# Kernel optimization log

Measured on AMD Instinct MI355X. Metric: run time of the kernel, lower is better.

## Reference

```python
import jax, jax.numpy as jnp
import numpy as np

D_K = 128
SCALE = float(np.sqrt(D_K))

def setup_inputs() -> dict:
    key = jax.random.key(0)
    k1, k2, k3, k4 = jax.random.split(key, 4)
    B, S, D = 16, 2048, 128
    Q = jax.random.normal(k1, (B, S, D), dtype=jnp.float32)
    K = jax.random.normal(k2, (B, S, D), dtype=jnp.float32)
    V = jax.random.normal(k3, (B, S, D), dtype=jnp.float32)
    mask = jax.random.randint(k4, (B, 1, S), 0, 2).astype(jnp.bool_)
    return {"Q": Q, "K": K, "V": V, "mask": mask}

def reference(Q, K, V, mask):
    # scores: (B, Sq, Sk)
    scores = jnp.einsum("bqd,bkd->bqk", Q, K) / SCALE
    allow = jnp.broadcast_to(mask, scores.shape)
    neg = jnp.finfo(scores.dtype).min
    scores = jnp.where(allow, scores, neg)
    query_has_keys = jnp.any(allow, axis=-1, keepdims=True)  # (B, Sq, 1)
    scores = jnp.where(query_has_keys, scores, 0.0)
    attn_weights = jax.nn.softmax(scores, axis=-1)
    attn_weights = jnp.where(allow, attn_weights, 0.0)
    # dropout p=0.0 -> identity
    output = jnp.einsum("bqk,bkd->bqd", attn_weights, V)
    output = jnp.where(query_has_keys, output, 0.0)
    return output, attn_weights
```

## Files before the change

kernel.cpp:

```cpp
#include <hip/hip_runtime.h>

#define BB 16
#define SS 2048
#define DD 128
#define CE (0.08838834764831845f * 1.4426950408889634f)

typedef __attribute__((ext_vector_type(4))) float f32x4;
typedef __attribute__((ext_vector_type(8))) short short8;
typedef __attribute__((ext_vector_type(4))) unsigned short us4;
typedef __attribute__((ext_vector_type(8))) unsigned short us8;

__device__ inline unsigned short f2bf(float f) {
    unsigned u = __float_as_uint(f);
    u += 0x7fffu + ((u >> 16) & 1u);
    return (unsigned short)(u >> 16);
}

__device__ inline int swzA(int row, int col) {
    int byteoff = (row << 8) + ((col >> 3) << 4);
    byteoff ^= (row & 7) << 4;
    return (byteoff >> 1) + (col & 7);
}
__device__ inline int swzB(int row, int col) {
    int byteoff = (row << 7) + ((col >> 3) << 4);
    byteoff ^= (row & 7) << 4;
    return (byteoff >> 1) + (col & 7);
}

__global__ __launch_bounds__(256) void conv_bf16_kernel(
    const float* __restrict__ Q, const float* __restrict__ K,
    const int* __restrict__ mask,
    unsigned short* __restrict__ Qb, unsigned short* __restrict__ Kb,
    float* __restrict__ maskAdd)
{
    int idx = blockIdx.x * blockDim.x + threadIdx.x;
    const int total = BB * SS * DD / 4;
    for (int i = idx; i < total; i += gridDim.x * blockDim.x) {
        f32x4 q = reinterpret_cast<const f32x4*>(Q)[i];
        f32x4 k = reinterpret_cast<const f32x4*>(K)[i];
        us4 qh, kh;
        for (int j = 0; j < 4; ++j) { qh[j] = f2bf(q[j]); kh[j] = f2bf(k[j]); }
        reinterpret_cast<us4*>(Qb)[i] = qh;
        reinterpret_cast<us4*>(Kb)[i] = kh;
    }
    if (idx < BB * SS)
        maskAdd[idx] = mask[idx] ? 0.0f : __int_as_float(0xff800000);
}

__global__ __launch_bounds__(256) void vt_kernel(
    const float* __restrict__ V, unsigned short* __restrict__ VT)
{
    __shared__ unsigned short tile[64 * 136];
    int b = blockIdx.y, k0 = blockIdx.x << 6;
    int t = threadIdx.x;
    const float* Vg = V + ((size_t)b * SS + k0) * DD;
    for (int i = 0; i < 8; ++i) {
        int f4 = (i << 8) + t;
        int k  = f4 >> 5;
        int n  = (f4 & 31) << 2;
        f32x4 v = reinterpret_cast<const f32x4*>(Vg)[f4];
        us4 h;
        for (int j = 0; j < 4; ++j) h[j] = f2bf(v[j]);
        *reinterpret_cast<us4*>(&tile[k * 136 + n]) = h;
    }
    __syncthreads();
    unsigned short* outp = VT + (size_t)b * DD * SS;
    for (int i = 0; i < 4; ++i) {
        int id = (i << 8) + t;
        int n  = id >> 3;
        int c8 = id & 7;
        us8 o;
        for (int j = 0; j < 8; ++j) o[j] = tile[((c8 << 3) + j) * 136 + n];
        *reinterpret_cast<us8*>(&outp[(size_t)n * SS + k0 + (c8 << 3)]) = o;
    }
}

__global__ __launch_bounds__(256, 2) void flashA_kernel(
    const unsigned short* __restrict__ Qb, const unsigned short* __restrict__ Kb,
    const unsigned short* __restrict__ VT, const float* __restrict__ maskAdd,
    float* __restrict__ Op0, float* __restrict__ Op1, float* __restrict__ Lp)
{
    __shared__ unsigned short Ks[64 * 128];
    __shared__ unsigned short VTs[128 * 64];
    __shared__ unsigned short Ps[4 * 32 * 64];

    const int id = blockIdx.x;
    const int xcd = id & 7, j = id >> 3;
    const int b   = (xcd << 1) | (j >> 5);
    const int rem = j & 31;
    const int half = rem >> 4, qb = rem & 15;
    const int q0 = qb << 7;
    const int kvbase = half << 10;

    const int t = threadIdx.x, lane = t & 63, w = t >> 6;
    const int lr = lane & 15, lg = lane >> 4;

    const unsigned short* Kbb = Kb + (size_t)b * SS * DD;
    const unsigned short* Vbb = VT + (size_t)b * DD * SS;
    const float* Mb = maskAdd + (size_t)b * SS;

    const unsigned short* Qp = Qb + ((size_t)b * SS + q0 + w * 32) * DD;
    short8 qf[2][4];
    for (int m = 0; m < 2; ++m)
        for (int kb = 0; kb < 4; ++kb)
            qf[m][kb] = *reinterpret_cast<const short8*>(
                Qp + (size_t)(m * 16 + lr) * DD + kb * 32 + lg * 8);

    f32x4 oacc[2][8] = {};
    float rsum[2] = {0.f, 0.f};
    unsigned short* Pw = &Ps[w * 2048];

    us8 kstg[4], vstg[4];
    {
        for (int i = 0; i < 4; ++i) {
            int f = i * 256 + t;
            kstg[i] = *reinterpret_cast<const us8*>(
                Kbb + (size_t)(kvbase + (f >> 4)) * DD + ((f & 15) << 3));
            vstg[i] = *reinterpret_cast<const us8*>(
                Vbb + (size_t)(f >> 3) * SS + kvbase + ((f & 7) << 3));
        }
    }

    for (int kt = 0; kt < 16; ++kt) {
        const int kv0 = kvbase + (kt << 6);
        __syncthreads();
        for (int i = 0; i < 4; ++i) {
            int f = i * 256 + t;
            *reinterpret_cast<us8*>(&Ks[swzA(f >> 4, (f & 15) << 3)]) = kstg[i];
            *reinterpret_cast<us8*>(&VTs[swzB(f >> 3, (f & 7) << 3)]) = vstg[i];
        }
        __syncthreads();
        if (kt + 1 < 16) {
            int nb = kv0 + 64;
            for (int i = 0; i < 4; ++i) {
                int f = i * 256 + t;
                kstg[i] = *reinterpret_cast<const us8*>(
                    Kbb + (size_t)(nb + (f >> 4)) * DD + ((f & 15) << 3));
                vstg[i] = *reinterpret_cast<const us8*>(
                    Vbb + (size_t)(f >> 3) * SS + nb + ((f & 7) << 3));
            }
        }

        f32x4 sacc[2][4] = {};
        for (int kb = 0; kb < 4; ++kb) {
            short8 kf[4];
            for (int n = 0; n < 4; ++n)
                kf[n] = *reinterpret_cast<const short8*>(
                    &Ks[swzA(n * 16 + lr, kb * 32 + lg * 8)]);
            for (int n = 0; n < 4; ++n)
                for (int m = 0; m < 2; ++m)
                    sacc[m][n] = __builtin_amdgcn_mfma_f32_16x16x32_bf16(
                        kf[n], qf[m][kb], sacc[m][n], 0, 0, 0);
        }

        for (int n = 0; n < 4; ++n) {
            f32x4 ma = *reinterpret_cast<const f32x4*>(Mb + kv0 + n * 16 + lg * 4);
            for (int m = 0; m < 2; ++m) {
                us4 h;
                for (int r = 0; r < 4; ++r) {
                    float p = __builtin_amdgcn_exp2f(fmaf(sacc[m][n][r], CE, ma[r]));
                    rsum[m] += p;
                    h[r] = f2bf(p);
                }
                *reinterpret_cast<us4*>(&Pw[swzB(m * 16 + lr, n * 16 + lg * 4)]) = h;
            }
        }
        asm volatile("s_waitcnt lgkmcnt(0)" ::: "memory");
        __builtin_amdgcn_sched_barrier(0);

        for (int k2 = 0; k2 < 2; ++k2) {
            short8 pf[2];
            for (int m = 0; m < 2; ++m)
                pf[m] = *reinterpret_cast<const short8*>(
                    &Pw[swzB(m * 16 + lr, k2 * 32 + lg * 8)]);
            for (int nd = 0; nd < 8; ++nd) {
                short8 vf = *reinterpret_cast<const short8*>(
                    &VTs[swzB(nd * 16 + lr, k2 * 32 + lg * 8)]);
                for (int m = 0; m < 2; ++m)
                    oacc[m][nd] = __builtin_amdgcn_mfma_f32_16x16x32_bf16(
                        pf[m], vf, oacc[m][nd], 0, 0, 0);
            }
        }
    }

    for (int m = 0; m < 2; ++m) {
        rsum[m] += __shfl_xor(rsum[m], 16, 64);
        rsum[m] += __shfl_xor(rsum[m], 32, 64);
    }
    if (lane < 16)
        for (int m = 0; m < 2; ++m)
            Lp[(size_t)half * BB * SS + (size_t)b * SS + q0 + w * 32 + m * 16 + lane] = rsum[m];

    float* Op = half ? Op1 : Op0;
    float* Og = Op + ((size_t)b * SS + q0 + w * 32) * DD;
    for (int m = 0; m < 2; ++m)
        for (int nd = 0; nd < 8; ++nd)
            for (int r = 0; r < 4; ++r)
                Og[(size_t)(m * 16 + lg * 4 + r) * DD + nd * 16 + lr] = oacc[m][nd][r];
}

__global__ __launch_bounds__(256) void combine_kernel(
    const float* __restrict__ Op0, const float* __restrict__ Op1,
    const float* __restrict__ Lp, float* __restrict__ O, float* __restrict__ l2il)
{
    int i = blockIdx.x * 256 + threadIdx.x;
    int row = i >> 5;
    float L = Lp[row] + Lp[BB * SS + row];
    float il = L > 0.f ? 1.f / L : 0.f;
    f32x4 a = reinterpret_cast<const f32x4*>(Op0)[i];
    f32x4 c = reinterpret_cast<const f32x4*>(Op1)[i];
    f32x4 o;
    for (int r = 0; r < 4; ++r) o[r] = (a[r] + c[r]) * il;
    reinterpret_cast<f32x4*>(O)[i] = o;
    if ((i & 31) == 0)
        l2il[row] = L > 0.f ? -__builtin_amdgcn_logf(L) : __int_as_float(0xff800000);
}

__global__ __launch_bounds__(256, 4) void pstore_kernel(
    const unsigned short* __restrict__ Qb, const unsigned short* __restrict__ Kb,
    const float* __restrict__ maskAdd, const float* __restrict__ l2il,
    float* __restrict__ P)
{
    __shared__ unsigned short Ks[64 * 128];

    const int id = blockIdx.x;
    const int xcd = id & 7, j = id >> 3;
    const int b   = (xcd << 1) | (j >> 6);
    const int rem = j & 63;
    const int kvq = rem >> 4, qb = rem & 15;
    const int q0 = qb << 7, kvbase = kvq << 9;

    const int t = threadIdx.x, lane = t & 63, w = t >> 6;
    const int lr = lane & 15, lg = lane >> 4;

    const unsigned short* Kbb = Kb + (size_t)b * SS * DD;
    const float* Mb = maskAdd + (size_t)b * SS;

    const unsigned short* Qp = Qb + ((size_t)b * SS + q0 + w * 32) * DD;
    short8 qf[2][4];
    for (int m = 0; m < 2; ++m)
        for (int kb = 0; kb < 4; ++kb)
            qf[m][kb] = *reinterpret_cast<const short8*>(
                Qp + (size_t)(m * 16 + lr) * DD + kb * 32 + lg * 8);

    float lil[2];
    for (int m = 0; m < 2; ++m)
        lil[m] = l2il[(size_t)b * SS + q0 + w * 32 + m * 16 + lr];

    us8 kstg[4];
    for (int i = 0; i < 4; ++i) {
        int f = i * 256 + t;
        kstg[i] = *reinterpret_cast<const us8*>(
            Kbb + (size_t)(kvbase + (f >> 4)) * DD + ((f & 15) << 3));
    }

    for (int kt = 0; kt < 8; ++kt) {
        const int kv0 = kvbase + (kt << 6);
        __syncthreads();
        for (int i = 0; i < 4; ++i) {
            int f = i * 256 + t;
            *reinterpret_cast<us8*>(&Ks[swzA(f >> 4, (f & 15) << 3)]) = kstg[i];
        }
        __syncthreads();
        if (kt + 1 < 8) {
            int nb = kv0 + 64;
            for (int i = 0; i < 4; ++i) {
                int f = i * 256 + t;
                kstg[i] = *reinterpret_cast<const us8*>(
                    Kbb + (size_t)(nb + (f >> 4)) * DD + ((f & 15) << 3));
            }
        }

        f32x4 sacc[2][4] = {};
        for (int kb = 0; kb < 4; ++kb) {
            short8 kf[4];
            for (int n = 0; n < 4; ++n)
                kf[n] = *reinterpret_cast<const short8*>(
                    &Ks[swzA(n * 16 + lr, kb * 32 + lg * 8)]);
            for (int n = 0; n < 4; ++n)
                for (int m = 0; m < 2; ++m)
                    sacc[m][n] = __builtin_amdgcn_mfma_f32_16x16x32_bf16(
                        kf[n], qf[m][kb], sacc[m][n], 0, 0, 0);
        }

        for (int m = 0; m < 2; ++m) {
            float* Pp = P + ((size_t)b * SS + q0 + w * 32 + m * 16 + lr) * SS + kv0;
            for (int n = 0; n < 4; ++n) {
                f32x4 ma = *reinterpret_cast<const f32x4*>(Mb + kv0 + n * 16 + lg * 4);
                f32x4 out;
                for (int r = 0; r < 4; ++r)
                    out[r] = __builtin_amdgcn_exp2f(
                        fmaf(sacc[m][n][r], CE, ma[r]) + lil[m]);
                *reinterpret_cast<f32x4*>(Pp + n * 16 + lg * 4) = out;
            }
        }
    }
}

__global__ __launch_bounds__(256) void qk_exp_kernel(
    const float* __restrict__ Q, const float* __restrict__ Kin,
    const int* __restrict__ mask, float* __restrict__ P)
{
    __shared__ unsigned short Qs[128 * 128];
    __shared__ unsigned short Ks[128 * 128];
    const int b  = blockIdx.z;
    const int m0 = blockIdx.y << 7;
    const int n0 = blockIdx.x << 7;
    const int t  = threadIdx.x;
    const float* Qp = Q   + ((size_t)b * SS + m0) * DD;
    const float* Kp = Kin + ((size_t)b * SS + n0) * DD;
    for (int i = 0; i < 16; ++i) {
        int f4  = (i << 8) + t;
        int row = f4 >> 5;
        int col = (f4 & 31) << 2;
        f32x4 q = reinterpret_cast<const f32x4*>(Qp)[f4];
        f32x4 k = reinterpret_cast<const f32x4*>(Kp)[f4];
        us4 qh, kh;
        for (int jj = 0; jj < 4; ++jj) { qh[jj] = f2bf(q[jj]); kh[jj] = f2bf(k[jj]); }
        *reinterpret_cast<us4*>(&Qs[swzA(row, col)]) = qh;
        *reinterpret_cast<us4*>(&Ks[swzA(row, col)]) = kh;
    }
    __syncthreads();
    const int lane = t & 63, wid = t >> 6;
    const int wr = wid >> 1, wc = wid & 1;
    const int lr = lane & 15, lg = lane >> 4;
    f32x4 acc[4][4] = {};
    for (int kb = 0; kb < 4; ++kb) {
        short8 a[4], bq[4];
        int kcol = (kb << 5) + (lg << 3);
        for (int m = 0; m < 4; ++m)
            a[m] = *reinterpret_cast<const short8*>(&Qs[swzA((wr << 6) + (m << 4) + lr, kcol)]);
        for (int n = 0; n < 4; ++n)
            bq[n] = *reinterpret_cast<const short8*>(&Ks[swzA((wc << 6) + (n << 4) + lr, kcol)]);
        for (int m = 0; m < 4; ++m)
            for (int n = 0; n < 4; ++n)
                acc[m][n] = __builtin_amdgcn_mfma_f32_16x16x32_bf16(a[m], bq[n], acc[m][n], 0, 0, 0);
    }
    const int* am = mask + (size_t)b * SS;
    for (int n = 0; n < 4; ++n) {
        int col = n0 + (wc << 6) + (n << 4) + lr;
        bool allow = am[col] != 0;
        for (int m = 0; m < 4; ++m) {
            int rowb = m0 + (wr << 6) + (m << 4) + (lg << 2);
            float* Pp = P + ((size_t)b * SS + rowb) * SS + col;
            for (int r = 0; r < 4; ++r) {
                float p = allow ? __expf(acc[m][n][r] * 0.08838834764831845f) : 0.0f;
                Pp[(size_t)r * SS] = p;
            }
        }
    }
}

__global__ __launch_bounds__(256) void norm_kernel(float* __restrict__ P)
{
    int row  = (blockIdx.x << 2) + (threadIdx.x >> 6);
    int lane = threadIdx.x & 63;
    float* Pr = P + (size_t)row * SS;
    f32x4 v[8];
    float sum = 0.f;
    for (int i = 0; i < 8; ++i) {
        v[i] = reinterpret_cast<f32x4*>(Pr)[(i << 6) + lane];
        sum += v[i][0] + v[i][1] + v[i][2] + v[i][3];
    }
    for (int off = 1; off < 64; off <<= 1) sum += __shfl_xor(sum, off, 64);
    float inv = sum > 0.f ? 1.f / sum : 0.f;
    for (int i = 0; i < 8; ++i) {
        f32x4 wv = v[i];
        for (int jj = 0; jj < 4; ++jj) wv[jj] *= inv;
        reinterpret_cast<f32x4*>(Pr)[(i << 6) + lane] = wv;
    }
}

__global__ __launch_bounds__(256) void pv_fallback_kernel(
    const float* __restrict__ P, const float* __restrict__ V, float* __restrict__ O)
{
    __shared__ unsigned short Ws[64 * 64];
    const int b  = blockIdx.y;
    const int m0 = blockIdx.x << 6;
    const int t  = threadIdx.x, lane = t & 63, wid = t >> 6;
    const int wr = wid >> 1, wc = wid & 1;
    const int lr = lane & 15, lg = lane >> 4;
    const float* Pg = P + ((size_t)b * SS + m0) * SS;
    f32x4 acc[2][4] = {};
    for (int k0 = 0; k0 < SS; k0 += 64) {
        __syncthreads();
        for (int i = 0; i < 4; ++i) {
            int f4  = (i << 8) + t;
            int row = f4 >> 4;
            int col = (f4 & 15) << 2;
            f32x4 wv = *reinterpret_cast<const f32x4*>(Pg + (size_t)row * SS + k0 + col);
            us4 h;
            for (int jj = 0; jj < 4; ++jj) h[jj] = f2bf(wv[jj]);
            *reinterpret_cast<us4*>(&Ws[swzB(row, col)]) = h;
        }
        __syncthreads();
        for (int kk = 0; kk < 64; kk += 32) {
            short8 a[2], bv[4];
            int kcol = kk + (lg << 3);
            for (int m = 0; m < 2; ++m)
                a[m] = *reinterpret_cast<const short8*>(&Ws[swzB((wr << 5) + (m << 4) + lr, kcol)]);
            for (int n = 0; n < 4; ++n) {
                int col = (wc << 6) + (n << 4) + lr;
                const float* vp = V + ((size_t)b * SS + k0 + kcol) * DD + col;
                short8 x;
                for (int jj = 0; jj < 8; ++jj) x[jj] = (short)f2bf(vp[(size_t)jj * DD]);
                bv[n] = x;
            }
            for (int m = 0; m < 2; ++m)
                for (int n = 0; n < 4; ++n)
                    acc[m][n] = __builtin_amdgcn_mfma_f32_16x16x32_bf16(a[m], bv[n], acc[m][n], 0, 0, 0);
        }
    }
    float* Og = O + ((size_t)b * SS + m0) * DD;
    for (int m = 0; m < 2; ++m)
        for (int n = 0; n < 4; ++n)
            for (int r = 0; r < 4; ++r)
                Og[(size_t)((wr << 5) + (m << 4) + (lg << 2) + r) * DD
                   + (wc << 6) + (n << 4) + lr] = acc[m][n][r];
}

extern "C" void kernel_launch(void* const* d_in, const int* in_sizes, int n_in,
                              void* d_out, int out_size, void* d_ws, size_t ws_size,
                              hipStream_t stream)
{
    const float* Q  = (const float*)d_in[0];
    const float* K  = (const float*)d_in[1];
    const float* V  = (const float*)d_in[2];
    const int* mask = (const int*)d_in[3];
    float* O = (float*)d_out;
    float* P = O + (size_t)BB * SS * DD;

    const size_t nE = (size_t)BB * SS * DD;
    const size_t need = 3 * nE * sizeof(unsigned short)
                      + 4 * (size_t)BB * SS * sizeof(float) + 256;

    if (ws_size >= need) {
        unsigned short* Qb = (unsigned short*)d_ws;
        unsigned short* Kb = Qb + nE;
        unsigned short* VT = Kb + nE;
        float* maskAdd = (float*)(VT + nE);
        float* Lp      = maskAdd + (size_t)BB * SS;
        float* l2il    = Lp + 2 * (size_t)BB * SS;
        float* Op0 = P;
        float* Op1 = P + nE;

        conv_bf16_kernel<<<1024, 256, 0, stream>>>(Q, K, mask, Qb, Kb, maskAdd);
        vt_kernel<<<dim3(SS / 64, BB), 256, 0, stream>>>(V, VT);
        flashA_kernel<<<512, 256, 0, stream>>>(Qb, Kb, VT, maskAdd, Op0, Op1, Lp);
        combine_kernel<<<4096, 256, 0, stream>>>(Op0, Op1, Lp, O, l2il);
        pstore_kernel<<<1024, 256, 0, stream>>>(Qb, Kb, maskAdd, l2il, P);
    } else {
        qk_exp_kernel<<<dim3(SS / 128, SS / 128, BB), 256, 0, stream>>>(Q, K, mask, P);
        norm_kernel<<<(BB * SS) / 4, 256, 0, stream>>>(P);
        pv_fallback_kernel<<<dim3(SS / 64, BB), 256, 0, stream>>>(P, V, O);
    }
}
```

Measured before the change: 143.9 us.

## Double-buffer K/V shared tiles, fuse prep kernels, and split P staging

Merges the Q/K bf16 conversion, mask preparation and V transpose into one prep kernel, removing a launch. In the flash and P-store kernels, K/V tiles are now double-buffered in shared memory, so the next tile is written during compute and one barrier per iteration is dropped. The flash kernel also processes P in two 32-column halves through a smaller per-wave buffer and raises wave priority around the MFMA sections. In exchange, shared memory use grows, which may lower occupancy.

```diff
diff --git a/kernel.cpp b/kernel.cpp
--- a/kernel.cpp
+++ b/kernel.cpp
@@ -27,38 +27,35 @@
     return (byteoff >> 1) + (col & 7);
 }
 
-__global__ __launch_bounds__(256) void conv_bf16_kernel(
+__global__ __launch_bounds__(256) void prep_kernel(
     const float* __restrict__ Q, const float* __restrict__ K,
-    const int* __restrict__ mask,
+    const float* __restrict__ V, const int* __restrict__ mask,
     unsigned short* __restrict__ Qb, unsigned short* __restrict__ Kb,
-    float* __restrict__ maskAdd)
-{
-    int idx = blockIdx.x * blockDim.x + threadIdx.x;
-    const int total = BB * SS * DD / 4;
-    for (int i = idx; i < total; i += gridDim.x * blockDim.x) {
-        f32x4 q = reinterpret_cast<const f32x4*>(Q)[i];
-        f32x4 k = reinterpret_cast<const f32x4*>(K)[i];
-        us4 qh, kh;
-        for (int j = 0; j < 4; ++j) { qh[j] = f2bf(q[j]); kh[j] = f2bf(k[j]); }
-        reinterpret_cast<us4*>(Qb)[i] = qh;
-        reinterpret_cast<us4*>(Kb)[i] = kh;
-    }
-    if (idx < BB * SS)
-        maskAdd[idx] = mask[idx] ? 0.0f : __int_as_float(0xff800000);
-}
-
-__global__ __launch_bounds__(256) void vt_kernel(
-    const float* __restrict__ V, unsigned short* __restrict__ VT)
+    unsigned short* __restrict__ VT, float* __restrict__ maskAdd)
 {
     __shared__ unsigned short tile[64 * 136];
     int b = blockIdx.y, k0 = blockIdx.x << 6;
     int t = threadIdx.x;
-    const float* Vg = V + ((size_t)b * SS + k0) * DD;
+    const size_t base = ((size_t)b * SS + k0) * DD;
+
+    for (int i = 0; i < 8; ++i) {
+        int f4 = (i << 8) + t;
+        f32x4 q = reinterpret_cast<const f32x4*>(Q + base)[f4];
+        f32x4 k = reinterpret_cast<const f32x4*>(K + base)[f4];
+        us4 qh, kh;
+        for (int j = 0; j < 4; ++j) { qh[j] = f2bf(q[j]); kh[j] = f2bf(k[j]); }
+        reinterpret_cast<us4*>(Qb + base)[f4] = qh;
+        reinterpret_cast<us4*>(Kb + base)[f4] = kh;
+    }
+    if (t < 64)
+        maskAdd[(size_t)b * SS + k0 + t] =
+            mask[(size_t)b * SS + k0 + t] ? 0.0f : __int_as_float(0xff800000);
+
     for (int i = 0; i < 8; ++i) {
         int f4 = (i << 8) + t;
         int k  = f4 >> 5;
         int n  = (f4 & 31) << 2;
-        f32x4 v = reinterpret_cast<const f32x4*>(Vg)[f4];
+        f32x4 v = reinterpret_cast<const f32x4*>(V + base)[f4];
         us4 h;
         for (int j = 0; j < 4; ++j) h[j] = f2bf(v[j]);
         *reinterpret_cast<us4*>(&tile[k * 136 + n]) = h;
@@ -80,9 +77,9 @@
     const unsigned short* __restrict__ VT, const float* __restrict__ maskAdd,
     float* __restrict__ Op0, float* __restrict__ Op1, float* __restrict__ Lp)
 {
-    __shared__ unsigned short Ks[64 * 128];
-    __shared__ unsigned short VTs[128 * 64];
-    __shared__ unsigned short Ps[4 * 32 * 64];
+    __shared__ unsigned short Ks[2][64 * 128];
+    __shared__ unsigned short VTs[2][128 * 64];
+    __shared__ unsigned short Ps[4 * 1024];
 
     const int id = blockIdx.x;
     const int xcd = id & 7, j = id >> 3;
@@ -108,80 +105,82 @@
 
     f32x4 oacc[2][8] = {};
     float rsum[2] = {0.f, 0.f};
-    unsigned short* Pw = &Ps[w * 2048];
+    unsigned short* Pw = &Ps[w * 1024];
 
     us8 kstg[4], vstg[4];
-    {
-        for (int i = 0; i < 4; ++i) {
-            int f = i * 256 + t;
-            kstg[i] = *reinterpret_cast<const us8*>(
-                Kbb + (size_t)(kvbase + (f >> 4)) * DD + ((f & 15) << 3));
-            vstg[i] = *reinterpret_cast<const us8*>(
-                Vbb + (size_t)(f >> 3) * SS + kvbase + ((f & 7) << 3));
-        }
-    }
+#define LOADTILE(kv)                                                             \
+    for (int i = 0; i < 4; ++i) {                                                \
+        int f = i * 256 + t;                                                     \
+        kstg[i] = *reinterpret_cast<const us8*>(                                 \
+            Kbb + (size_t)((kv) + (f >> 4)) * DD + ((f & 15) << 3));             \
+        vstg[i] = *reinterpret_cast<const us8*>(                                 \
+            Vbb + (size_t)(f >> 3) * SS + (kv) + ((f & 7) << 3));                \
+    }
+#define WRITETILE(bf)                                                            \
+    for (int i = 0; i < 4; ++i) {                                                \
+        int f = i * 256 + t;                                                     \
+        *reinterpret_cast<us8*>(&Ks[bf][swzA(f >> 4, (f & 15) << 3)]) = kstg[i]; \
+        *reinterpret_cast<us8*>(&VTs[bf][swzB(f >> 3, (f & 7) << 3)]) = vstg[i]; \
+    }
+
+    LOADTILE(kvbase);
+    WRITETILE(0);
 
     for (int kt = 0; kt < 16; ++kt) {
+        const int cur = kt & 1;
         const int kv0 = kvbase + (kt << 6);
+        if (kt + 1 < 16) { LOADTILE(kv0 + 64); }
         __syncthreads();
-        for (int i = 0; i < 4; ++i) {
-            int f = i * 256 + t;
-            *reinterpret_cast<us8*>(&Ks[swzA(f >> 4, (f & 15) << 3)]) = kstg[i];
-            *reinterpret_cast<us8*>(&VTs[swzB(f >> 3, (f & 7) << 3)]) = vstg[i];
-        }
-        __syncthreads();
-        if (kt + 1 < 16) {
-            int nb = kv0 + 64;
-            for (int i = 0; i < 4; ++i) {
-                int f = i * 256 + t;
-                kstg[i] = *reinterpret_cast<const us8*>(
-                    Kbb + (size_t)(nb + (f >> 4)) * DD + ((f & 15) << 3));
-                vstg[i] = *reinterpret_cast<const us8*>(
-                    Vbb + (size_t)(f >> 3) * SS + nb + ((f & 7) << 3));
-            }
-        }
 
         f32x4 sacc[2][4] = {};
+        __builtin_amdgcn_s_setprio(1);
         for (int kb = 0; kb < 4; ++kb) {
             short8 kf[4];
             for (int n = 0; n < 4; ++n)
                 kf[n] = *reinterpret_cast<const short8*>(
-                    &Ks[swzA(n * 16 + lr, kb * 32 + lg * 8)]);
+                    &Ks[cur][swzA(n * 16 + lr, kb * 32 + lg * 8)]);
             for (int n = 0; n < 4; ++n)
                 for (int m = 0; m < 2; ++m)
                     sacc[m][n] = __builtin_amdgcn_mfma_f32_16x16x32_bf16(
                         kf[n], qf[m][kb], sacc[m][n], 0, 0, 0);
         }
-
-        for (int n = 0; n < 4; ++n) {
-            f32x4 ma = *reinterpret_cast<const f32x4*>(Mb + kv0 + n * 16 + lg * 4);
-            for (int m = 0; m < 2; ++m) {
-                us4 h;
-                for (int r = 0; r < 4; ++r) {
-                    float p = __builtin_amdgcn_exp2f(fmaf(sacc[m][n][r], CE, ma[r]));
-                    rsum[m] += p;
-                    h[r] = f2bf(p);
+        __builtin_amdgcn_s_setprio(0);
+
+        for (int h = 0; h < 2; ++h) {
+            for (int nl = 0; nl < 2; ++nl) {
+                int n = h * 2 + nl;
+                f32x4 ma = *reinterpret_cast<const f32x4*>(Mb + kv0 + n * 16 + lg * 4);
+                for (int m = 0; m < 2; ++m) {
+                    us4 hh;
+                    for (int r = 0; r < 4; ++r) {
+                        float p = __builtin_amdgcn_exp2f(fmaf(sacc[m][n][r], CE, ma[r]));
+                        rsum[m] += p;
+                        hh[r] = f2bf(p);
+                    }
+                    *reinterpret_cast<us4*>(&Pw[swzB(lr, m * 32 + nl * 16 + lg * 4)]) = hh;
                 }
-                *reinterpret_cast<us4*>(&Pw[swzB(m * 16 + lr, n * 16 + lg * 4)]) = h;
             }
-        }
-        asm volatile("s_waitcnt lgkmcnt(0)" ::: "memory");
-        __builtin_amdgcn_sched_barrier(0);
-
-        for (int k2 = 0; k2 < 2; ++k2) {
+            asm volatile("s_waitcnt lgkmcnt(0)" ::: "memory");
+            __builtin_amdgcn_sched_barrier(0);
+
             short8 pf[2];
             for (int m = 0; m < 2; ++m)
-                pf[m] = *reinterpret_cast<const short8*>(
-                    &Pw[swzB(m * 16 + lr, k2 * 32 + lg * 8)]);
+                pf[m] = *reinterpret_cast<const short8*>(&Pw[swzB(lr, m * 32 + lg * 8)]);
+            __builtin_amdgcn_s_setprio(1);
             for (int nd = 0; nd < 8; ++nd) {
                 short8 vf = *reinterpret_cast<const short8*>(
-                    &VTs[swzB(nd * 16 + lr, k2 * 32 + lg * 8)]);
+                    &VTs[cur][swzB(nd * 16 + lr, h * 32 + lg * 8)]);
                 for (int m = 0; m < 2; ++m)
                     oacc[m][nd] = __builtin_amdgcn_mfma_f32_16x16x32_bf16(
                         pf[m], vf, oacc[m][nd], 0, 0, 0);
             }
-        }
-    }
+            __builtin_amdgcn_s_setprio(0);
+        }
+
+        if (kt + 1 < 16) { WRITETILE(cur ^ 1); }
+    }
+#undef LOADTILE
+#undef WRITETILE
 
     for (int m = 0; m < 2; ++m) {
         rsum[m] += __shfl_xor(rsum[m], 16, 64);
@@ -221,7 +220,7 @@
     const float* __restrict__ maskAdd, const float* __restrict__ l2il,
     float* __restrict__ P)
 {
-    __shared__ unsigned short Ks[64 * 128];
+    __shared__ unsigned short Ks[2][64 * 128];
 
     const int id = blockIdx.x;
     const int xcd = id & 7, j = id >> 3;
@@ -248,35 +247,33 @@
         lil[m] = l2il[(size_t)b * SS + q0 + w * 32 + m * 16 + lr];
 
     us8 kstg[4];
-    for (int i = 0; i < 4; ++i) {
-        int f = i * 256 + t;
-        kstg[i] = *reinterpret_cast<const us8*>(
-            Kbb + (size_t)(kvbase + (f >> 4)) * DD + ((f & 15) << 3));
-    }
+#define LOADK(kv)                                                                \
+    for (int i = 0; i < 4; ++i) {                                                \
+        int f = i * 256 + t;                                                     \
+        kstg[i] = *reinterpret_cast<const us8*>(                                 \
+            Kbb + (size_t)((kv) + (f >> 4)) * DD + ((f & 15) << 3));             \
+    }
+#define WRITEK(bf)                                                               \
+    for (int i = 0; i < 4; ++i) {                                                \
+        int f = i * 256 + t;                                                     \
+        *reinterpret_cast<us8*>(&Ks[bf][swzA(f >> 4, (f & 15) << 3)]) = kstg[i]; \
+    }
+
+    LOADK(kvbase);
+    WRITEK(0);
 
     for (int kt = 0; kt < 8; ++kt) {
+        const int cur = kt & 1;
         const int kv0 = kvbase + (kt << 6);
+        if (kt + 1 < 8) { LOADK(kv0 + 64); }
         __syncthreads();
-        for (int i = 0; i < 4; ++i) {
-            int f = i * 256 + t;
-            *reinterpret_cast<us8*>(&Ks[swzA(f >> 4, (f & 15) << 3)]) = kstg[i];
-        }
-        __syncthreads();
-        if (kt + 1 < 8) {
-            int nb = kv0 + 64;
-            for (int i = 0; i < 4; ++i) {
-                int f = i * 256 + t;
-                kstg[i] = *reinterpret_cast<const us8*>(
-                    Kbb + (size_t)(nb + (f >> 4)) * DD + ((f & 15) << 3));
-            }
-        }
 
         f32x4 sacc[2][4] = {};
         for (int kb = 0; kb < 4; ++kb) {
             short8 kf[4];
             for (int n = 0; n < 4; ++n)
                 kf[n] = *reinterpret_cast<const short8*>(
-                    &Ks[swzA(n * 16 + lr, kb * 32 + lg * 8)]);
+                    &Ks[cur][swzA(n * 16 + lr, kb * 32 + lg * 8)]);
             for (int n = 0; n < 4; ++n)
                 for (int m = 0; m < 2; ++m)
                     sacc[m][n] = __builtin_amdgcn_mfma_f32_16x16x32_bf16(
@@ -294,7 +291,11 @@
                 *reinterpret_cast<f32x4*>(Pp + n * 16 + lg * 4) = out;
             }
         }
-    }
+
+        if (kt + 1 < 8) { WRITEK(cur ^ 1); }
+    }
+#undef LOADK
+#undef WRITEK
 }
 
 __global__ __launch_bounds__(256) void qk_exp_kernel(
@@ -444,8 +445,7 @@
         float* Op0 = P;
         float* Op1 = P + nE;
 
-        conv_bf16_kernel<<<1024, 256, 0, stream>>>(Q, K, mask, Qb, Kb, maskAdd);
-        vt_kernel<<<dim3(SS / 64, BB), 256, 0, stream>>>(V, VT);
+        prep_kernel<<<dim3(SS / 64, BB), 256, 0, stream>>>(Q, K, V, mask, Qb, Kb, VT, maskAdd);
         flashA_kernel<<<512, 256, 0, stream>>>(Qb, Kb, VT, maskAdd, Op0, Op1, Lp);
         combine_kernel<<<4096, 256, 0, stream>>>(Op0, Op1, Lp, O, l2il);
         pstore_kernel<<<1024, 256, 0, stream>>>(Qb, Kb, maskAdd, l2il, P);
```

Measured after the change: 138.8 us. -3.6%, faster.
